# Performance work log

Measured on AMD Instinct MI355X. Metric: run time of the kernel, lower is better.

Reference implementation:

```python
import jax, jax.numpy as jnp
import numpy as np

N_NODES = 50000


def _gcn_conv(x, W, b, src, dst, n_nodes):
    """PyG GCNConv: add self-loops, D^-1/2 (A+I) D^-1/2 X W + b."""
    loop = jnp.arange(n_nodes, dtype=src.dtype)
    src_f = jnp.concatenate([src, loop])  # [E+N]
    dst_f = jnp.concatenate([dst, loop])
    # degree over destination nodes (edge weight 1, incl. self loops)
    deg = jax.ops.segment_sum(jnp.ones_like(dst_f, dtype=x.dtype), dst_f,
                              num_segments=n_nodes)
    dinv = jnp.where(deg > 0, jax.lax.rsqrt(deg), 0.0)
    norm = dinv[src_f] * dinv[dst_f]  # [E+N]
    h = x @ W  # [N, C_out] dense GEMM first (C_out <= C_in here)
    msg = h[src_f] * norm[:, None]  # gather + scale
    out = jax.ops.segment_sum(msg, dst_f, num_segments=n_nodes)
    return out + b


def setup_inputs() -> dict:
    key = jax.random.key(0)
    k1, k2, k3, k4, k5, k6 = jax.random.split(key, 6)
    in_c, hid_c, out_c = 512, 512, 40
    x = jax.random.normal(k1, (N_NODES, in_c), dtype=jnp.float32)
    edge_index = jax.random.randint(k2, (2, 800000), 0, N_NODES, dtype=jnp.int64)
    # Glorot-style init for the linear weights, zero bias (PyG default)
    W1 = jax.random.normal(k3, (in_c, hid_c), dtype=jnp.float32) / np.sqrt(in_c)
    b1 = jnp.zeros((hid_c,), dtype=jnp.float32)
    W2 = jax.random.normal(k4, (hid_c, out_c), dtype=jnp.float32) / np.sqrt(hid_c)
    b2 = jnp.zeros((out_c,), dtype=jnp.float32)
    return {"x": x, "edge_index": edge_index, "W1": W1, "b1": b1,
            "W2": W2, "b2": b2}


def reference(x, edge_index, W1, b1, W2, b2):
    src, dst = edge_index[0], edge_index[1]
    h = _gcn_conv(x, W1, b1, src, dst, N_NODES)
    h = jax.nn.relu(h)
    h = _gcn_conv(h, W2, b2, src, dst, N_NODES)
    return jax.nn.log_softmax(h, axis=1)
```

## Files before the change

### kernel.cpp

```cpp
#include <hip/hip_runtime.h>


typedef unsigned int u32;
typedef unsigned short u16;
typedef unsigned long long u64;
typedef __bf16 bf16x8 __attribute__((ext_vector_type(8)));
typedef float f32x4 __attribute__((ext_vector_type(4)));
typedef u32 u32x4 __attribute__((ext_vector_type(4)));

#define C_IN 512
#define C_HID 512
#define C_OUT 40
#define H_SCALE 24.0f
#define H_INV_SCALE (1.0f / 24.0f)

__device__ __forceinline__ float bf2f(u16 u) {
    u32 x = ((u32)u) << 16;
    return __builtin_bit_cast(float, x);
}
__device__ __forceinline__ u16 f2bf(float f) {
    u32 x = __builtin_bit_cast(u32, f);
    x += 0x7fffu + ((x >> 16) & 1u);
    return (u16)(x >> 16);
}
__device__ __forceinline__ char q8(float v) {
    float c = fminf(fmaxf(v * H_SCALE, -127.f), 127.f);
    return (char)__float2int_rn(c);
}
__device__ __forceinline__ u32 pk2(float a, float b) {
    u16 lo = __builtin_bit_cast(u16, (__bf16)a);
    u16 hi = __builtin_bit_cast(u16, (__bf16)b);
    return (u32)lo | ((u32)hi << 16);
}
__device__ __forceinline__ u32x4 pk8(float4 a, float4 b) {
    u32x4 r;
    r.x = pk2(a.x, a.y); r.y = pk2(a.z, a.w);
    r.z = pk2(b.x, b.y); r.w = pk2(b.z, b.w);
    return r;
}
__host__ __device__ __forceinline__ int imin(int a, int b) { return a < b ? a : b; }
__host__ __device__ __forceinline__ int imax(int a, int b) { return a > b ? a : b; }

__device__ __forceinline__ float ldf(const void* p, int i, int isbf) {
    return isbf ? bf2f(((const u16*)p)[i]) : ((const float*)p)[i];
}

__global__ __launch_bounds__(256) void k_initprep(
    const u32* __restrict__ x32, const int* __restrict__ ei,
    const void* __restrict__ W1, const void* __restrict__ b1,
    const void* __restrict__ W2, const void* __restrict__ b2,
    int* flags, int* deg, int* cursor, u64* state,
    u16* __restrict__ w1t, u16* __restrict__ w2t,
    float* __restrict__ b1f, float* __restrict__ b2f,
    int n, int nchunks) {
    __shared__ float tile[64][65];
    __shared__ int s_flags[2];
    int tid = threadIdx.x;
    if (tid < 64) {
        int lane = tid;
        int z = (ei[2 * lane + 1] == 0) ? 1 : 0;
        u32 e = (x32[lane] >> 7) & 0xff;
        int v = (e >= 110 && e <= 133) ? 1 : 0;
        unsigned long long bz = __ballot(z);
        unsigned long long bv = __ballot(v);
        if (lane == 0) {
            s_flags[0] = (__popcll(bz) == 64) ? 2 : 1;
            s_flags[1] = (__popcll(bv) >= 48) ? 1 : 0;
        }
    }
    __syncthreads();
    int isbf = s_flags[1];
    int i0 = blockIdx.x * 256 + tid;
    int stride = gridDim.x * 256;
    if (blockIdx.x == 0 && tid == 0) { flags[0] = s_flags[0]; flags[1] = isbf; }
    if (i0 < n) { deg[i0] = 1; cursor[i0] = 0; }
    if (i0 < nchunks) state[i0] = 0ULL;
    if (blockIdx.x < 64) {
        int t = blockIdx.x;
        int tr = t >> 3, tc = t & 7;
        int rr = tid >> 2, cq = (tid & 3) * 16;
#pragma unroll
        for (int c = 0; c < 16; ++c)
            tile[cq + c][rr] = ldf(W1, (tr * 64 + rr) * 512 + tc * 64 + cq + c, isbf);
        __syncthreads();
#pragma unroll
        for (int c = 0; c < 16; ++c)
            w1t[(size_t)(tc * 64 + rr) * 512 + tr * 64 + cq + c] = f2bf(tile[rr][cq + c]);
    }
    for (int i = i0; i < 64 * 512; i += stride) {
        int nn = i >> 9, k = i & 511;
        w2t[i] = (nn < C_OUT) ? f2bf(ldf(W2, k * C_OUT + nn, isbf)) : (u16)0;
    }
    if (i0 < C_HID) b1f[i0] = ldf(b1, i0, isbf);
    if (i0 < C_OUT) b2f[i0] = ldf(b2, i0, isbf);
}

__global__ void k_deg(const int* __restrict__ ei, const int* __restrict__ flags,
                      int* deg, int E, int ecap, int n) {
    int e = blockIdx.x * 256 + threadIdx.x;
    if (e >= E) return;
    int st = flags[0];
    int cap = ecap * st - 1;
    u32 d = (u32)ei[imin((E + e) * st, cap)];
    if (d < (u32)n) atomicAdd(&deg[d], 1);
}

__global__ __launch_bounds__(256) void k_scan(
    const int* __restrict__ deg, float* __restrict__ dinv, int* __restrict__ offs,
    u64* state, int n, int nchunks) {
    __shared__ int sh[256];
    __shared__ int s_prefix;
    int tid = threadIdx.x;
    int c = blockIdx.x;
    int i = c * 256 + tid;
    int dv = (i < n) ? deg[i] : 1;
    if (i < n) dinv[i] = rsqrtf((float)imax(dv, 1));
    int v = (i < n) ? dv - 1 : 0;
    sh[tid] = v;
    __syncthreads();
    for (int d = 1; d < 256; d <<= 1) {
        int add = (tid >= d) ? sh[tid - d] : 0;
        __syncthreads();
        sh[tid] += add;
        __syncthreads();
    }
    int total = sh[255];
    if (tid == 0) {
        atomicExch(&state[c], (1ULL << 62) | (u64)(u32)total);
        long long prefix = 0;
        int cc = c - 1;
        while (cc >= 0) {
            u64 s;
            do { s = atomicAdd(&state[cc], 0ULL); } while (s == 0ULL);
            prefix += (long long)(u32)s;
            if (s >> 63) break;
            --cc;
        }
        atomicExch(&state[c], (1ULL << 63) | (u64)(u32)(prefix + total));
        s_prefix = (int)prefix;
        if (c == nchunks - 1) offs[n] = (int)(prefix + total);
    }
    __syncthreads();
    int pfx = s_prefix;
    if (i < n) offs[i] = pfx + sh[tid] - v;
}

__global__ void k_sort(const int* __restrict__ ei, const int* __restrict__ flags,
                       const int* __restrict__ offs, int* cursor, int* csr,
                       int E, int ecap, int n) {
    int e = blockIdx.x * 256 + threadIdx.x;
    if (e >= E) return;
    int st = flags[0];
    int cap = ecap * st - 1;
    u32 d = (u32)ei[imin((E + e) * st, cap)];
    u32 s = (u32)ei[imin(e * st, cap)];
    if (d < (u32)n && s < (u32)n) {
        int pos = offs[d] + atomicAdd(&cursor[(int)d], 1);
        if ((u32)pos < (u32)E) csr[pos] = (int)s;
    }
}

typedef __attribute__((address_space(1))) const u32 glds_src;
typedef __attribute__((address_space(3))) u32 glds_dst;

__global__ __launch_bounds__(256) void k_gemm128(
    const u16* __restrict__ xbf, const float* __restrict__ xf32,
    const int* __restrict__ flags, const u16* __restrict__ Bt,
    char* __restrict__ C, int M, int K, int ldc) {
    int isbf = flags[1];
    __shared__ __align__(16) u16 As0[64 * 32], As1[64 * 32];
    __shared__ __align__(16) u16 Bs0[128 * 32], Bs1[128 * 32];
    int tid = threadIdx.x;
    int wave = tid >> 6, lane = tid & 63;
    int quad = lane >> 4, lrow = lane & 15;
    int wrow = (wave & 1) * 32, wcol = (wave >> 1) * 64;

    int nwg = gridDim.x;
    int id = blockIdx.x;
    int q = nwg >> 3, r = nwg & 7;
    int xcd = id & 7, j8 = id >> 3;
    int wg = (xcd < r ? xcd * (q + 1) : r * (q + 1) + (xcd - r) * q) + j8;
    int row0 = (wg >> 2) * 64;
    int n0 = (wg & 3) * 128;

    int lr = lane >> 2;
    int lc = (lane & 3) * 8;
    int ar = row0 + wave * 16 + lr;
    int br = n0 + wave * 32 + lr;
    u16* As0_w = As0 + (wave * 16) * 32;
    u16* As1_w = As1 + (wave * 16) * 32;
    u16* Bs0_w = Bs0 + (wave * 32) * 32;
    u16* Bs1_w = Bs1 + (wave * 32) * 32;

    f32x4 acc[2][4] = {};
    int kTiles = K >> 6;
    for (int kt = 0; kt < kTiles; ++kt) {
        int k0 = kt * 64;
        int a0 = imin(ar, M - 1);
        if (isbf) {
            const u16* gA0 = xbf + (size_t)a0 * K + k0 + lc;
            __builtin_amdgcn_global_load_lds((glds_src*)gA0, (glds_dst*)As0_w, 16, 0, 0);
            __builtin_amdgcn_global_load_lds((glds_src*)(gA0 + 32), (glds_dst*)As1_w, 16, 0, 0);
        } else {
            const float* f0 = xf32 + (size_t)a0 * K + k0 + lc;
            float4 u0 = *(const float4*)(f0);
            float4 u1 = *(const float4*)(f0 + 4);
            float4 u2 = *(const float4*)(f0 + 32);
            float4 u3 = *(const float4*)(f0 + 36);
            *(u32x4*)(As0_w + lr * 32 + lc) = pk8(u0, u1);
            *(u32x4*)(As1_w + lr * 32 + lc) = pk8(u2, u3);
        }
        const u16* gB0 = Bt + (size_t)br * K + k0 + lc;
        const u16* gB1 = Bt + (size_t)(br + 16) * K + k0 + lc;
        __builtin_amdgcn_global_load_lds((glds_src*)gB0, (glds_dst*)Bs0_w, 16, 0, 0);
        __builtin_amdgcn_global_load_lds((glds_src*)gB1, (glds_dst*)(Bs0_w + 16 * 32), 16, 0, 0);
        __builtin_amdgcn_global_load_lds((glds_src*)(gB0 + 32), (glds_dst*)Bs1_w, 16, 0, 0);
        __builtin_amdgcn_global_load_lds((glds_src*)(gB1 + 32), (glds_dst*)(Bs1_w + 16 * 32), 16, 0, 0);
        __syncthreads();
#pragma unroll
        for (int ko = 0; ko < 2; ++ko) {
            const u16* Asrc = ko ? As1 : As0;
            const u16* Bsrc = ko ? Bs1 : Bs0;
            bf16x8 af[2], bfr[4];
#pragma unroll
            for (int i = 0; i < 2; ++i)
                af[i] = *(const bf16x8*)(Asrc + (wrow + i * 16 + lrow) * 32 + quad * 8);
#pragma unroll
            for (int j = 0; j < 4; ++j)
                bfr[j] = *(const bf16x8*)(Bsrc + (wcol + j * 16 + lrow) * 32 + quad * 8);
#pragma unroll
            for (int i = 0; i < 2; ++i)
#pragma unroll
                for (int j = 0; j < 4; ++j)
                    acc[i][j] = __builtin_amdgcn_mfma_f32_16x16x32_bf16(af[i], bfr[j],
                                                                        acc[i][j], 0, 0, 0);
        }
        __syncthreads();
    }
#pragma unroll
    for (int i = 0; i < 2; ++i)
#pragma unroll
        for (int j = 0; j < 4; ++j)
#pragma unroll
            for (int r2 = 0; r2 < 4; ++r2) {
                int row = row0 + wrow + i * 16 + quad * 4 + r2;
                int col = n0 + wcol + j * 16 + lrow;
                if (row < M) C[(size_t)row * ldc + col] = q8(acc[i][j][r2]);
            }
}

#define B2ROW 520
__global__ __launch_bounds__(256) void k_gemm64(
    const u16* __restrict__ A, const u16* __restrict__ Bt, u16* __restrict__ Cout,
    int M, int K, int Ncols, int ldc) {
    __shared__ __align__(16) u16 Bsh[48 * B2ROW];
    int tid = threadIdx.x;
    int wave = tid >> 6, lane = tid & 63;
    int quad = lane >> 4, lrow = lane & 15;

    for (int i = tid; i < 48 * 64; i += 256) {
        int rw = i >> 6, cv = (i & 63) * 8;
        *(uint4*)(Bsh + rw * B2ROW + cv) = *(const uint4*)(Bt + (size_t)rw * 512 + cv);
    }
    __syncthreads();

    int row0 = blockIdx.x * 128 + wave * 32;
    int r0 = imin(row0 + lrow, M - 1);
    int r1 = imin(row0 + 16 + lrow, M - 1);
    const u16* a0p = A + (size_t)r0 * K + quad * 8;
    const u16* a1p = A + (size_t)r1 * K + quad * 8;
    const u16* b0p = Bsh + (0 * 16 + lrow) * B2ROW + quad * 8;
    const u16* b1p = Bsh + (1 * 16 + lrow) * B2ROW + quad * 8;
    const u16* b2p = Bsh + (2 * 16 + lrow) * B2ROW + quad * 8;

    f32x4 c00 = {}, c01 = {}, c02 = {};
    f32x4 c10 = {}, c11 = {}, c12 = {};
#pragma unroll 4
    for (int k0 = 0; k0 < C_HID; k0 += 32) {
        bf16x8 a0 = *(const bf16x8*)(a0p + k0);
        bf16x8 a1 = *(const bf16x8*)(a1p + k0);
        bf16x8 b0 = *(const bf16x8*)(b0p + k0);
        bf16x8 b1 = *(const bf16x8*)(b1p + k0);
        bf16x8 b2 = *(const bf16x8*)(b2p + k0);
        c00 = __builtin_amdgcn_mfma_f32_16x16x32_bf16(a0, b0, c00, 0, 0, 0);
        c01 = __builtin_amdgcn_mfma_f32_16x16x32_bf16(a0, b1, c01, 0, 0, 0);
        c02 = __builtin_amdgcn_mfma_f32_16x16x32_bf16(a0, b2, c02, 0, 0, 0);
        c10 = __builtin_amdgcn_mfma_f32_16x16x32_bf16(a1, b0, c10, 0, 0, 0);
        c11 = __builtin_amdgcn_mfma_f32_16x16x32_bf16(a1, b1, c11, 0, 0, 0);
        c12 = __builtin_amdgcn_mfma_f32_16x16x32_bf16(a1, b2, c12, 0, 0, 0);
    }
    f32x4 cc[2][3] = {{c00, c01, c02}, {c10, c11, c12}};
#pragma unroll
    for (int i = 0; i < 2; ++i)
#pragma unroll
        for (int t = 0; t < 3; ++t)
#pragma unroll
            for (int r = 0; r < 4; ++r) {
                int row = row0 + i * 16 + quad * 4 + r;
                int col = t * 16 + lrow;
                if (row < M && col < Ncols)
                    Cout[(size_t)row * ldc + col] = f2bf(cc[i][t][r]);
            }
}

__device__ __forceinline__ void accum8i(float* acc, uint2 p, float w) {
    int lo = (int)p.x, hi = (int)p.y;
    acc[0] += w * (float)(signed char)(lo);
    acc[1] += w * (float)(signed char)(lo >> 8);
    acc[2] += w * (float)(signed char)(lo >> 16);
    acc[3] += w * (float)(signed char)(lo >> 24);
    acc[4] += w * (float)(signed char)(hi);
    acc[5] += w * (float)(signed char)(hi >> 8);
    acc[6] += w * (float)(signed char)(hi >> 16);
    acc[7] += w * (float)(signed char)(hi >> 24);
}

__global__ __launch_bounds__(256) void k_agg1(
    const char* __restrict__ hq, const int* __restrict__ csr, const int* __restrict__ offs,
    const float* __restrict__ dinv, const float* __restrict__ b1f,
    u16* __restrict__ out, int n, int Etot) {
    int wave = threadIdx.x >> 6, lane = threadIdx.x & 63;
    int v = blockIdx.x * 4 + wave;
    if (v >= n) return;
    float dv = dinv[v];
    float wself = dv * dv * H_INV_SCALE;

    float acc[8] = {0.f, 0.f, 0.f, 0.f, 0.f, 0.f, 0.f, 0.f};
    uint2 hs = *(const uint2*)(hq + (size_t)v * C_HID + lane * 8);
    accum8i(acc, hs, wself);

    int e0 = imax(0, imin(offs[v], Etot));
    int e1 = imax(e0, imin(offs[v + 1], Etot));
    for (int base = e0; base < e1; base += 64) {
        int cnt = imin(64, e1 - base);
        int sreg = 0; float wreg = 0.f;
        if (lane < cnt) {
            u32 s = (u32)csr[base + lane];
            s = (s < (u32)n) ? s : 0u;
            sreg = (int)s;
            wreg = dv * dinv[s] * H_INV_SCALE;
        }
        int j = 0;
        for (; j + 16 <= cnt; j += 16) {
            int ss[16]; float ww[16]; uint2 pp[16];
#pragma unroll
            for (int t = 0; t < 16; ++t) {
                ss[t] = __shfl(sreg, j + t);
                ww[t] = __shfl(wreg, j + t);
            }
#pragma unroll
            for (int t = 0; t < 16; ++t)
                pp[t] = *(const uint2*)(hq + (size_t)ss[t] * C_HID + lane * 8);
#pragma unroll
            for (int t = 0; t < 16; ++t) accum8i(acc, pp[t], ww[t]);
        }
        for (; j + 8 <= cnt; j += 8) {
            int ss[8]; float ww[8]; uint2 pp[8];
#pragma unroll
            for (int t = 0; t < 8; ++t) {
                ss[t] = __shfl(sreg, j + t);
                ww[t] = __shfl(wreg, j + t);
            }
#pragma unroll
            for (int t = 0; t < 8; ++t)
                pp[t] = *(const uint2*)(hq + (size_t)ss[t] * C_HID + lane * 8);
#pragma unroll
            for (int t = 0; t < 8; ++t) accum8i(acc, pp[t], ww[t]);
        }
        for (; j + 4 <= cnt; j += 4) {
            int ss[4]; float ww[4]; uint2 pp[4];
#pragma unroll
            for (int t = 0; t < 4; ++t) {
                ss[t] = __shfl(sreg, j + t);
                ww[t] = __shfl(wreg, j + t);
            }
#pragma unroll
            for (int t = 0; t < 4; ++t)
                pp[t] = *(const uint2*)(hq + (size_t)ss[t] * C_HID + lane * 8);
#pragma unroll
            for (int t = 0; t < 4; ++t) accum8i(acc, pp[t], ww[t]);
        }
        for (; j < cnt; ++j) {
            int sj = __shfl(sreg, j);
            float wj = __shfl(wreg, j);
            uint2 pj = *(const uint2*)(hq + (size_t)sj * C_HID + lane * 8);
            accum8i(acc, pj, wj);
        }
    }

    float4 ba = *(const float4*)(b1f + lane * 8);
    float4 bb = *(const float4*)(b1f + lane * 8 + 4);
    float r0 = fmaxf(acc[0] + ba.x, 0.f), r1 = fmaxf(acc[1] + ba.y, 0.f);
    float r2 = fmaxf(acc[2] + ba.z, 0.f), r3 = fmaxf(acc[3] + ba.w, 0.f);
    float r4 = fmaxf(acc[4] + bb.x, 0.f), r5 = fmaxf(acc[5] + bb.y, 0.f);
    float r6 = fmaxf(acc[6] + bb.z, 0.f), r7 = fmaxf(acc[7] + bb.w, 0.f);
    u32x4 o;
    o.x = (u32)f2bf(r0) | ((u32)f2bf(r1) << 16);
    o.y = (u32)f2bf(r2) | ((u32)f2bf(r3) << 16);
    o.z = (u32)f2bf(r4) | ((u32)f2bf(r5) << 16);
    o.w = (u32)f2bf(r6) | ((u32)f2bf(r7) << 16);
    __builtin_nontemporal_store(o, (u32x4*)(out + (size_t)v * C_HID + lane * 8));
}

__global__ __launch_bounds__(256) void k_agg2(
    const u16* __restrict__ h2, const int* __restrict__ csr, const int* __restrict__ offs,
    const float* __restrict__ dinv, const float* __restrict__ b2f,
    const int* __restrict__ flags, void* __restrict__ out, int n, int Etot) {
    int wave = threadIdx.x >> 6, lane = threadIdx.x & 63;
    int v = blockIdx.x * 4 + wave;
    if (v >= n) return;
    float dv = dinv[v];

    int g = lane / 10;
    int f4 = lane - g * 10;
    bool active = (g < 6);

    float4 acc = make_float4(0.f, 0.f, 0.f, 0.f);
    if (g == 0) {
        uint2 pv = *(const uint2*)(h2 + (size_t)v * C_OUT + f4 * 4);
        float w = dv * dv;
        acc.x = w * bf2f((u16)pv.x); acc.y = w * bf2f((u16)(pv.x >> 16));
        acc.z = w * bf2f((u16)pv.y); acc.w = w * bf2f((u16)(pv.y >> 16));
    }

    int e0 = imax(0, imin(offs[v], Etot));
    int e1 = imax(e0, imin(offs[v + 1], Etot));
    for (int base = e0; base < e1; base += 64) {
        int cnt = imin(64, e1 - base);
        int sreg = 0; float wreg = 0.f;
        if (lane < cnt) {
            u32 s = (u32)csr[base + lane];
            s = (s < (u32)n) ? s : 0u;
            sreg = (int)s;
            wreg = dv * dinv[s];
        }
        for (int j = 0; j < cnt; j += 24) {
            uint2 p[4]; float w4[4];
#pragma unroll
            for (int t = 0; t < 4; ++t) {
                int jj = j + t * 6 + g;
                int idx = imin(jj, cnt - 1);
                int sj = __shfl(sreg, idx);
                float wj = __shfl(wreg, idx);
                w4[t] = (active && jj < cnt) ? wj : 0.f;
                p[t] = make_uint2(0, 0);
                if (active) p[t] = *(const uint2*)(h2 + (size_t)sj * C_OUT + f4 * 4);
            }
#pragma unroll
            for (int t = 0; t < 4; ++t) {
                acc.x += w4[t] * bf2f((u16)p[t].x);
                acc.y += w4[t] * bf2f((u16)(p[t].x >> 16));
                acc.z += w4[t] * bf2f((u16)p[t].y);
                acc.w += w4[t] * bf2f((u16)(p[t].y >> 16));
            }
        }
    }

    float4 t;
    t.x = __shfl(acc.x, lane + 30); t.y = __shfl(acc.y, lane + 30);
    t.z = __shfl(acc.z, lane + 30); t.w = __shfl(acc.w, lane + 30);
    if (lane < 30) { acc.x += t.x; acc.y += t.y; acc.z += t.z; acc.w += t.w; }
    float4 t1, t2;
    t1.x = __shfl(acc.x, lane + 10); t1.y = __shfl(acc.y, lane + 10);
    t1.z = __shfl(acc.z, lane + 10); t1.w = __shfl(acc.w, lane + 10);
    t2.x = __shfl(acc.x, lane + 20); t2.y = __shfl(acc.y, lane + 20);
    t2.z = __shfl(acc.z, lane + 20); t2.w = __shfl(acc.w, lane + 20);
    if (lane < 10) {
        acc.x += t1.x + t2.x; acc.y += t1.y + t2.y;
        acc.z += t1.z + t2.z; acc.w += t1.w + t2.w;
        acc.x += b2f[f4 * 4 + 0]; acc.y += b2f[f4 * 4 + 1];
        acc.z += b2f[f4 * 4 + 2]; acc.w += b2f[f4 * 4 + 3];
    }

    float m = -1e30f;
    if (lane < 10) m = fmaxf(fmaxf(acc.x, acc.y), fmaxf(acc.z, acc.w));
    for (int off = 32; off > 0; off >>= 1) m = fmaxf(m, __shfl_xor(m, off));
    float s = 0.f;
    if (lane < 10)
        s = expf(acc.x - m) + expf(acc.y - m) + expf(acc.z - m) + expf(acc.w - m);
    for (int off = 32; off > 0; off >>= 1) s += __shfl_xor(s, off);
    if (lane < 10) {
        float ls = m + logf(s);
        if (flags[1]) {
            ushort4 o;
            o.x = f2bf(acc.x - ls); o.y = f2bf(acc.y - ls);
            o.z = f2bf(acc.z - ls); o.w = f2bf(acc.w - ls);
            *(ushort4*)((u16*)out + (size_t)v * C_OUT + f4 * 4) = o;
        } else {
            float4 o = make_float4(acc.x - ls, acc.y - ls, acc.z - ls, acc.w - ls);
            *(float4*)((float*)out + (size_t)v * C_OUT + f4 * 4) = o;
        }
    }
}


extern "C" void kernel_launch(void* const* d_in, const int* in_sizes, int n_in,
                              void* d_out, int out_size, void* d_ws, size_t ws_size,
                              hipStream_t stream) {
    const void* x = d_in[0];
    const int* ei = (const int*)d_in[1];
    const void* W1 = d_in[2];
    const void* b1 = d_in[3];
    const void* W2 = d_in[4];
    const void* b2 = d_in[5];

    const int N = out_size / C_OUT;
    const int Mx = in_sizes[0] / C_IN;
    const int M = (N < Mx) ? N : Mx;
    const int ECAP = in_sizes[1];
    const int E = ECAP / 2;

    char* p = (char*)d_ws;
    size_t used = 0;
    auto carve = [&](size_t bytes) -> void* {
        void* r = (void*)p;
        size_t b = (bytes + 255) & ~(size_t)255;
        p += b; used += b;
        return r;
    };
    int* flags = (int*)carve(256);
    int* deg = (int*)carve((size_t)N * 4);
    int* cursor = (int*)carve((size_t)N * 4);
    float* dinv = (float*)carve((size_t)N * 4);
    int* offs = (int*)carve((size_t)(N + 1) * 4);
    u64* state = (u64*)carve(4096);
    int* csr = (int*)carve((size_t)E * 4);
    u16* w1t = (u16*)carve((size_t)C_HID * C_IN * 2);
    u16* w2t = (u16*)carve((size_t)64 * C_HID * 2);
    float* b1f = (float*)carve(C_HID * 4);
    float* b2f = (float*)carve(256);
    u16* bufA = (u16*)carve((size_t)N * C_HID * 2);
    u16* bufB = (u16*)carve((size_t)N * C_HID * 2);
    if (used > ws_size) return;

    char* h_i8 = (char*)bufB;
    u16* hagg = bufA;
    u16* h2 = bufB;

    const int NB = (N + 255) / 256;
    const int EB = (E + 255) / 256;

    k_initprep<<<NB, 256, 0, stream>>>((const u32*)x, ei, W1, b1, W2, b2,
                                       flags, deg, cursor, state,
                                       w1t, w2t, b1f, b2f, N, NB);
    k_deg<<<EB, 256, 0, stream>>>(ei, flags, deg, E, ECAP, N);
    k_scan<<<NB, 256, 0, stream>>>(deg, dinv, offs, state, N, NB);
    k_sort<<<EB, 256, 0, stream>>>(ei, flags, offs, cursor, csr, E, ECAP, N);

    int nbx = (M + 63) / 64;
    k_gemm128<<<nbx * 4, 256, 0, stream>>>((const u16*)x, (const float*)x, flags,
                                           w1t, h_i8, M, C_IN, C_HID);

    k_agg1<<<(N + 3) / 4, 256, 0, stream>>>(h_i8, csr, offs, dinv, b1f, hagg, N, E);

    k_gemm64<<<(M + 127) / 128, 256, 0, stream>>>(hagg, w2t, h2, N, C_HID, C_OUT, C_OUT);

    k_agg2<<<(N + 3) / 4, 256, 0, stream>>>(h2, csr, offs, dinv, b2f, flags, d_out, N, E);
}
```

Baseline: 399.0 us.

## Load A fragments directly into registers and swizzle B tiles in LDS

The first-layer GEMM now has each wave read its A-operand MFMA fragments straight from global memory into registers, converting fp32 to bf16 in place, rather than staging A through shared memory. B tiles still go through LDS, but with an XOR swizzle on the column chunk to reduce bank conflicts on fragment reads. This removes LDS traffic and LDS space for A. In exchange, the two column-wave pairs each load the same A rows, which doubles A global reads and relies on caches to absorb them.

```diff
diff --git a/kernel.cpp b/kernel.cpp
--- a/kernel.cpp
+++ b/kernel.cpp
@@ -32,11 +32,11 @@
     u16 hi = __builtin_bit_cast(u16, (__bf16)b);
     return (u32)lo | ((u32)hi << 16);
 }
-__device__ __forceinline__ u32x4 pk8(float4 a, float4 b) {
+__device__ __forceinline__ bf16x8 pkfrag(float4 a, float4 b) {
     u32x4 r;
     r.x = pk2(a.x, a.y); r.y = pk2(a.z, a.w);
     r.z = pk2(b.x, b.y); r.w = pk2(b.z, b.w);
-    return r;
+    return __builtin_bit_cast(bf16x8, r);
 }
 __host__ __device__ __forceinline__ int imin(int a, int b) { return a < b ? a : b; }
 __host__ __device__ __forceinline__ int imax(int a, int b) { return a > b ? a : b; }
@@ -168,7 +168,6 @@
     const int* __restrict__ flags, const u16* __restrict__ Bt,
     char* __restrict__ C, int M, int K, int ldc) {
     int isbf = flags[1];
-    __shared__ __align__(16) u16 As0[64 * 32], As1[64 * 32];
     __shared__ __align__(16) u16 Bs0[128 * 32], Bs1[128 * 32];
     int tid = threadIdx.x;
     int wave = tid >> 6, lane = tid & 63;
@@ -184,56 +183,71 @@
     int n0 = (wg & 3) * 128;
 
     int lr = lane >> 2;
-    int lc = (lane & 3) * 8;
-    int ar = row0 + wave * 16 + lr;
+    int lcq = lane & 3;
+    int skey = (lr >> 1) & 3;
+    int sc = (lcq ^ skey) * 8;
     int br = n0 + wave * 32 + lr;
-    u16* As0_w = As0 + (wave * 16) * 32;
-    u16* As1_w = As1 + (wave * 16) * 32;
     u16* Bs0_w = Bs0 + (wave * 32) * 32;
     u16* Bs1_w = Bs1 + (wave * 32) * 32;
+    const u16* gB0b = Bt + (size_t)br * K + sc;
+    const u16* gB1b = Bt + (size_t)(br + 16) * K + sc;
+
+    int r0i = imin(row0 + wrow + lrow, M - 1);
+    int r1i = imin(row0 + wrow + 16 + lrow, M - 1);
+    const u16* aB0 = xbf + (size_t)r0i * K + quad * 8;
+    const u16* aB1 = xbf + (size_t)r1i * K + quad * 8;
+    const float* aF0 = xf32 + (size_t)r0i * K + quad * 8;
+    const float* aF1 = xf32 + (size_t)r1i * K + quad * 8;
+
+    int bkey = (lrow >> 1) & 3;
+    int bq = (quad ^ bkey) * 8;
 
     f32x4 acc[2][4] = {};
     int kTiles = K >> 6;
     for (int kt = 0; kt < kTiles; ++kt) {
         int k0 = kt * 64;
-        int a0 = imin(ar, M - 1);
+        __builtin_amdgcn_global_load_lds((glds_src*)(gB0b + k0), (glds_dst*)Bs0_w, 16, 0, 0);
+        __builtin_amdgcn_global_load_lds((glds_src*)(gB1b + k0), (glds_dst*)(Bs0_w + 16 * 32), 16, 0, 0);
+        __builtin_amdgcn_global_load_lds((glds_src*)(gB0b + k0 + 32), (glds_dst*)Bs1_w, 16, 0, 0);
+        __builtin_amdgcn_global_load_lds((glds_src*)(gB1b + k0 + 32), (glds_dst*)(Bs1_w + 16 * 32), 16, 0, 0);
+        bf16x8 a00, a10, a01, a11;
         if (isbf) {
-            const u16* gA0 = xbf + (size_t)a0 * K + k0 + lc;
-            __builtin_amdgcn_global_load_lds((glds_src*)gA0, (glds_dst*)As0_w, 16, 0, 0);
-            __builtin_amdgcn_global_load_lds((glds_src*)(gA0 + 32), (glds_dst*)As1_w, 16, 0, 0);
+            a00 = *(const bf16x8*)(aB0 + k0);
+            a10 = *(const bf16x8*)(aB1 + k0);
+            a01 = *(const bf16x8*)(aB0 + k0 + 32);
+            a11 = *(const bf16x8*)(aB1 + k0 + 32);
         } else {
-            const float* f0 = xf32 + (size_t)a0 * K + k0 + lc;
-            float4 u0 = *(const float4*)(f0);
-            float4 u1 = *(const float4*)(f0 + 4);
-            float4 u2 = *(const float4*)(f0 + 32);
-            float4 u3 = *(const float4*)(f0 + 36);
-            *(u32x4*)(As0_w + lr * 32 + lc) = pk8(u0, u1);
-            *(u32x4*)(As1_w + lr * 32 + lc) = pk8(u2, u3);
-        }
-        const u16* gB0 = Bt + (size_t)br * K + k0 + lc;
-        const u16* gB1 = Bt + (size_t)(br + 16) * K + k0 + lc;
-        __builtin_amdgcn_global_load_lds((glds_src*)gB0, (glds_dst*)Bs0_w, 16, 0, 0);
-        __builtin_amdgcn_global_load_lds((glds_src*)gB1, (glds_dst*)(Bs0_w + 16 * 32), 16, 0, 0);
-        __builtin_amdgcn_global_load_lds((glds_src*)(gB0 + 32), (glds_dst*)Bs1_w, 16, 0, 0);
-        __builtin_amdgcn_global_load_lds((glds_src*)(gB1 + 32), (glds_dst*)(Bs1_w + 16 * 32), 16, 0, 0);
+            float4 u0 = *(const float4*)(aF0 + k0);
+            float4 u1 = *(const float4*)(aF0 + k0 + 4);
+            float4 u2 = *(const float4*)(aF1 + k0);
+            float4 u3 = *(const float4*)(aF1 + k0 + 4);
+            float4 u4 = *(const float4*)(aF0 + k0 + 32);
+            float4 u5 = *(const float4*)(aF0 + k0 + 36);
+            float4 u6 = *(const float4*)(aF1 + k0 + 32);
+            float4 u7 = *(const float4*)(aF1 + k0 + 36);
+            a00 = pkfrag(u0, u1);
+            a10 = pkfrag(u2, u3);
+            a01 = pkfrag(u4, u5);
+            a11 = pkfrag(u6, u7);
+        }
         __syncthreads();
 #pragma unroll
         for (int ko = 0; ko < 2; ++ko) {
-            const u16* Asrc = ko ? As1 : As0;
             const u16* Bsrc = ko ? Bs1 : Bs0;
-            bf16x8 af[2], bfr[4];
-#pragma unroll
-            for (int i = 0; i < 2; ++i)
-                af[i] = *(const bf16x8*)(Asrc + (wrow + i * 16 + lrow) * 32 + quad * 8);
+            bf16x8 aA = ko ? a01 : a00;
+            bf16x8 aBv = ko ? a11 : a10;
+            bf16x8 bfr[4];
 #pragma unroll
             for (int j = 0; j < 4; ++j)
-                bfr[j] = *(const bf16x8*)(Bsrc + (wcol + j * 16 + lrow) * 32 + quad * 8);
-#pragma unroll
-            for (int i = 0; i < 2; ++i)
-#pragma unroll
-                for (int j = 0; j < 4; ++j)
-                    acc[i][j] = __builtin_amdgcn_mfma_f32_16x16x32_bf16(af[i], bfr[j],
-                                                                        acc[i][j], 0, 0, 0);
+                bfr[j] = *(const bf16x8*)(Bsrc + (wcol + j * 16 + lrow) * 32 + bq);
+#pragma unroll
+            for (int j = 0; j < 4; ++j)
+                acc[0][j] = __builtin_amdgcn_mfma_f32_16x16x32_bf16(aA, bfr[j],
+                                                                    acc[0][j], 0, 0, 0);
+#pragma unroll
+            for (int j = 0; j < 4; ++j)
+                acc[1][j] = __builtin_amdgcn_mfma_f32_16x16x32_bf16(aBv, bfr[j],
+                                                                    acc[1][j], 0, 0, 0);
         }
         __syncthreads();
     }
```

Result: slower. 462.8 us (+16.0%).
